# Performance work log

Hardware: AMD Instinct MI355X
Metric: run time of the kernel (lower is better)

## Reference

```python
import jax, jax.numpy as jnp
import numpy as np

K = 3  # n_neighbors


def setup_inputs() -> dict:
    key = jax.random.key(0)
    k1, k2, k3 = jax.random.split(key, 3)
    N, D, C, B = 400000, 27, 11, 512  # train size, 3*N_PEAKS_MAX, classes, query batch
    train_features = jax.random.normal(k1, (N, D), dtype=jnp.float32)
    label_idx = jax.random.randint(k2, (N,), 0, C)
    train_labels = jax.nn.one_hot(label_idx, C, dtype=jnp.float32)
    query = jax.random.normal(k3, (B, D), dtype=jnp.float32)
    return {"query": query, "train_features": train_features, "train_labels": train_labels}


def _divide_no_nan(x, y):
    # tf.math.divide_no_nan: 0 where denominator is 0
    y_safe = jnp.where(y != 0, y, 1.0)
    return jnp.where(y != 0, x / y_safe, 0.0)


def reference(query, train_features, train_labels):
    # scale = per-feature max abs over training set (computed in __init__)
    scale = jnp.max(jnp.abs(train_features), axis=0)            # [D]
    train_s = _divide_no_nan(train_features, scale)             # [N,D]
    q_s = _divide_no_nan(query, scale)                          # [B,D]

    xn = jnp.sum(train_s * train_s, axis=1)                     # [N]
    qn = jnp.sum(q_s * q_s, axis=1)                             # [B]
    d2 = qn[:, None] - 2.0 * jnp.einsum('bd,nd->bn', q_s, train_s) + xn[None, :]
    dist = jnp.sqrt(jnp.maximum(d2, 0.0))                       # [B,N]

    neg_kd, idx = jax.lax.top_k(-dist, K)                       # k smallest distances
    kd = -neg_kd                                                # [B,K]

    lab = train_labels[idx]                                     # [B,K,C]
    # inverse-distance weighted vote (safe against zero distances)
    kd_safe = jnp.where(kd == 0.0, 1.0, kd)
    votes = jnp.sum(lab / kd_safe[:, :, None], axis=1)          # [B,C]
    vote_res = jax.nn.one_hot(jnp.argmax(votes, axis=1), train_labels.shape[1], dtype=jnp.float32)

    # exact-match branch: if the nearest distance is 0, return its label directly
    zero_hit = (jnp.min(kd, axis=1) == 0.0)[:, None]            # [B,1]
    result = jnp.where(zero_hit, lab[:, 0, :], vote_res)        # [B,C]
    return kd, result
```

## Files before the change

### kernel.cpp

```cpp
#include <hip/hip_runtime.h>
#include <math.h>

typedef _Float16 h8 __attribute__((ext_vector_type(8)));
typedef float    f4v __attribute__((ext_vector_type(4)));

#define N_TRAIN 400000
#define DIMS    27
#define BQ      512
#define NCLS    11
#define KNN     3
#define NB      500
#define P1T     1024
#define PTS_BLK 800
#define PTS_SUP 160
#define NSUP    5
#define NPT     10
#define RAWF    4320
#define TILE_B  2048
#define NC      (NB * KNN)
#define SB      1024
#define RPB     392
#define SROWS   128
#define P2T     512

#define U64MAX 0xFFFFFFFFFFFFFFFFULL

__global__ __launch_bounds__(256) void k_scale(const float* __restrict__ train,
                                               unsigned* __restrict__ scale_u) {
    __shared__ float st[SROWS * DIMS];
    __shared__ float sp[243];
    int tid = threadIdx.x;
    int r0 = blockIdx.x * RPB;
    int r1 = min(r0 + RPB, N_TRAIN);
    int c  = tid % DIMS;
    int rr = tid / DIMS;
    float m = 0.f;
    for (int base = r0; base < r1; base += SROWS) {
        int cnt = min(SROWS, r1 - base);
        int tot4 = (cnt * DIMS) >> 2;
        const uint4* src4 = (const uint4*)(train + (size_t)base * DIMS);
        uint4* st4 = (uint4*)st;
        for (int i = tid; i < tot4; i += 256) st4[i] = src4[i];
        __syncthreads();
        if (tid < 243) {
            for (int r = rr; r < cnt; r += 9)
                m = fmaxf(m, fabsf(st[r * DIMS + c]));
        }
        __syncthreads();
    }
    if (tid < 243) sp[tid] = m;
    __syncthreads();
    if (tid < DIMS) {
        float v = 0.f;
#pragma unroll
        for (int g = 0; g < 9; ++g) v = fmaxf(v, sp[g * DIMS + tid]);
        atomicMax(&scale_u[tid], __float_as_uint(v));
    }
}

__global__ __launch_bounds__(64) void k_qprep(const float* __restrict__ query,
                                              const unsigned* __restrict__ scale_u,
                                              _Float16* __restrict__ Qhi,
                                              _Float16* __restrict__ Qlo) {
    int q = blockIdx.x * 64 + threadIdx.x;
    if (q >= BQ) return;
    const float* r = query + (size_t)q * DIMS;
#pragma unroll
    for (int d = 0; d < 32; ++d) {
        _Float16 hi = (_Float16)0.f, lo = (_Float16)0.f;
        if (d < DIMS) {
            float sc = __uint_as_float(scale_u[d]);
            float inv = (sc != 0.f) ? 1.f / sc : 0.f;
            float xs = r[d] * inv;
            hi = (_Float16)xs;
            lo = (_Float16)(xs - (float)hi);
        } else if (d == 27) {
            hi = (_Float16)1.f;
        }
        Qhi[q * 32 + d] = hi;
        Qlo[q * 32 + d] = lo;
    }
}

__device__ __forceinline__ void insert3(float d, int i, float* bd, int* bi) {
    if (d < bd[2] || (d == bd[2] && i < bi[2])) {
        if (d < bd[1] || (d == bd[1] && i < bi[1])) {
            bd[2] = bd[1]; bi[2] = bi[1];
            if (d < bd[0] || (d == bd[0] && i < bi[0])) {
                bd[1] = bd[0]; bi[1] = bi[0];
                bd[0] = d; bi[0] = i;
            } else { bd[1] = d; bi[1] = i; }
        } else { bd[2] = d; bi[2] = i; }
    }
}

__device__ __forceinline__ unsigned long long shfl_xor_u64(unsigned long long v, int m) {
    unsigned lo = (unsigned)v, hi = (unsigned)(v >> 32);
    lo = __shfl_xor(lo, m, 64);
    hi = __shfl_xor(hi, m, 64);
    return ((unsigned long long)hi << 32) | lo;
}

__device__ __forceinline__ void ins3u64(unsigned long long e,
                                        unsigned long long& t0,
                                        unsigned long long& t1,
                                        unsigned long long& t2) {
    unsigned long long a  = e < t2 ? e : t2;
    unsigned long long n2 = t1 > a ? t1 : a;
    unsigned long long n1 = t1 < a ? t1 : a;
    t2 = n2;
    unsigned long long m1 = t0 > n1 ? t0 : n1;
    t0 = t0 < n1 ? t0 : n1;
    t1 = m1;
}

__device__ __forceinline__ void stage16(const float* g, float* l) {
    __builtin_amdgcn_global_load_lds((const __attribute__((address_space(1))) void*)g,
                                     (__attribute__((address_space(3))) void*)l, 16, 0, 0);
}

__global__ __attribute__((amdgpu_flat_work_group_size(P1T, P1T)))
__attribute__((amdgpu_waves_per_eu(4)))
void k_pass1(const float* __restrict__ train,
             const unsigned* __restrict__ scale_u,
             const _Float16* __restrict__ Qhi,
             const _Float16* __restrict__ Qlo,
             unsigned long long* __restrict__ cand) {
    __shared__ float s_inv[32];
    __shared__ __align__(16) float raw[2][RAWF];
    __shared__ __align__(16) unsigned char conv[NPT * TILE_B];

    int tid = threadIdx.x;
    if (tid < 32) {
        float sc = __uint_as_float(scale_u[tid]);
        s_inv[tid] = (sc != 0.f) ? 1.f / sc : 0.f;
    }
    int lane = tid & 63, w = tid >> 6;
    int l15 = lane & 15, quad = lane >> 4;

    h8 bhi[2], blo[2];
#pragma unroll
    for (int j = 0; j < 2; ++j) {
        int qt = w * 2 + j;
        size_t e = (size_t)(qt * 16 + l15) * 32 + quad * 8;
        bhi[j] = *(const h8*)(Qhi + e);
        blo[j] = *(const h8*)(Qlo + e);
    }

    unsigned kb0[2][4], kb1[2][4];
#pragma unroll
    for (int j = 0; j < 2; ++j)
#pragma unroll
        for (int r = 0; r < 4; ++r) { kb0[j][r] = 0u; kb1[j][r] = 0u; }

    int p0 = blockIdx.x * PTS_BLK;
    const float* gsup = train + (size_t)p0 * DIMS;

    {
        const float* gp = gsup; float* lp = raw[0];
        stage16(gp + tid * 4, lp + tid * 4);
        if (tid < 56) stage16(gp + 4096 + tid * 4, lp + 4096 + tid * 4);
    }

    for (int s = 0; s < NSUP; ++s) {
        __syncthreads();

        const float* rw = raw[s & 1];
        if (tid < PTS_SUP * 4) {
            int p = tid >> 2, gq = tid & 3;
            float x[8]; float part = 0.f;
#pragma unroll
            for (int i = 0; i < 8; ++i) {
                int d = gq * 8 + i;
                int dc = d < DIMS ? d : (DIMS - 1);
                float v = rw[p * DIMS + dc] * s_inv[d];
                x[i] = v;
                part = fmaf(v, v, part);
            }
            part += __shfl_xor(part, 1, 64);
            part += __shfl_xor(part, 2, 64);
            h8 hv, lv;
#pragma unroll
            for (int i = 0; i < 8; ++i) {
                _Float16 h = (_Float16)x[i];
                hv[i] = h;
                lv[i] = (_Float16)(x[i] - (float)h);
            }
            if (gq == 3) {
                float tt = -0.5f * part;
                _Float16 th = (_Float16)tt;
                hv[3] = th;
                lv[3] = (_Float16)(tt - (float)th);
            }
            unsigned char* dstb = conv + (p >> 4) * TILE_B + gq * 256 + (p & 15) * 16;
            *(h8*)dstb = hv;
            *(h8*)(dstb + 1024) = lv;
        }
        __syncthreads();

        if (s + 1 < NSUP) {
            const float* gp = gsup + (size_t)(s + 1) * RAWF;
            float* lp = raw[(s + 1) & 1];
            stage16(gp + tid * 4, lp + tid * 4);
            if (tid < 56) stage16(gp + 4096 + tid * 4, lp + 4096 + tid * 4);
        }

        for (int t = 0; t < NPT; ++t) {
            const unsigned char* basep = conv + t * TILE_B;
            h8 ahi = *(const h8*)(basep + lane * 16);
            h8 alo = *(const h8*)(basep + 1024 + lane * 16);
            unsigned ic = 63u - (unsigned)(s * NPT + t);
#pragma unroll
            for (int j = 0; j < 2; ++j) {
                f4v acc = {64.f, 64.f, 64.f, 64.f};
                acc = __builtin_amdgcn_mfma_f32_16x16x32_f16(alo, bhi[j], acc, 0, 0, 0);
                acc = __builtin_amdgcn_mfma_f32_16x16x32_f16(ahi, blo[j], acc, 0, 0, 0);
                acc = __builtin_amdgcn_mfma_f32_16x16x32_f16(ahi, bhi[j], acc, 0, 0, 0);
#pragma unroll
                for (int r = 0; r < 4; ++r) {
                    unsigned key = (__float_as_uint(acc[r]) & 0xFFFFFFC0u) | ic;
                    unsigned b0 = kb0[j][r];
                    unsigned m  = key < b0 ? key : b0;
                    kb0[j][r]   = key > b0 ? key : b0;
                    unsigned b1 = kb1[j][r];
                    kb1[j][r]   = m > b1 ? m : b1;
                }
            }
        }
    }

    int g = blockIdx.x;
    int qr4 = quad * 4;
#pragma unroll
    for (int j = 0; j < 2; ++j) {
        unsigned long long t0 = U64MAX, t1 = U64MAX, t2 = U64MAX;
#pragma unroll
        for (int r = 0; r < 4; ++r) {
#pragma unroll
            for (int h = 0; h < 2; ++h) {
                unsigned k = h ? kb1[j][r] : kb0[j][r];
                unsigned tile = 63u - (k & 63u);
                unsigned gi = (unsigned)(p0 + (int)tile * 16 + qr4 + r);
                unsigned long long e = ((unsigned long long)(~(k | 63u)) << 32) | gi;
                ins3u64(e, t0, t1, t2);
            }
        }
#pragma unroll
        for (int step = 16; step <= 32; step <<= 1) {
            unsigned long long o0 = shfl_xor_u64(t0, step);
            unsigned long long o1 = shfl_xor_u64(t1, step);
            unsigned long long o2 = shfl_xor_u64(t2, step);
            ins3u64(o0, t0, t1, t2);
            ins3u64(o1, t0, t1, t2);
            ins3u64(o2, t0, t1, t2);
        }
        if (quad == 0) {
            int qq = (w * 2 + j) * 16 + l15;
            size_t off = (size_t)qq * NC + (size_t)g * KNN;
            cand[off + 0] = t0; cand[off + 1] = t1; cand[off + 2] = t2;
        }
    }
}

#define CE(a, b) do { unsigned long long lo_ = (a) < (b) ? (a) : (b); \
                      unsigned long long hi_ = (a) < (b) ? (b) : (a); \
                      (a) = lo_; (b) = hi_; } while (0)

__global__ __launch_bounds__(P2T) void k_pass2(const unsigned long long* __restrict__ cand,
                                               const float* __restrict__ train,
                                               const float* __restrict__ query,
                                               const unsigned* __restrict__ scale_u,
                                               const float* __restrict__ labels,
                                               float* __restrict__ out) {
    __shared__ unsigned long long smerge[64];
    int q = blockIdx.x;
    int tid = threadIdx.x, lane = tid & 63, w = tid >> 6;
    const unsigned long long* cd = cand + (size_t)q * NC;

    unsigned long long c0 = cd[tid];
    unsigned long long c1 = cd[tid + P2T];
    unsigned long long c2 = (tid + 2 * P2T < NC) ? cd[tid + 2 * P2T] : U64MAX;
    CE(c0, c1); CE(c0, c2); CE(c1, c2);

#pragma unroll
    for (int k = 0; k < 8; ++k) {
        unsigned long long m = c0;
#pragma unroll
        for (int st = 1; st < 64; st <<= 1) {
            unsigned long long o = shfl_xor_u64(m, st);
            if (o < m) m = o;
        }
        if (lane == 0) smerge[w * 8 + k] = m;
        bool win = (c0 == m);
        c0 = win ? c1 : c0;
        c1 = win ? c2 : c1;
        c2 = win ? U64MAX : c2;
    }
    __syncthreads();
    if (w != 0) return;

    int myi = 0x7fffffff;
    {
        unsigned long long cur = smerge[lane];
#pragma unroll
        for (int k = 0; k < 8; ++k) {
            unsigned long long m = cur;
#pragma unroll
            for (int st = 1; st < 64; st <<= 1) {
                unsigned long long o = shfl_xor_u64(m, st);
                if (o < m) m = o;
            }
            if (lane == k) myi = (int)(unsigned)m;
            if (cur == m) cur = U64MAX;
        }
    }

    float inv[DIMS], qs_[DIMS], qn_ = 0.f;
#pragma unroll
    for (int d = 0; d < DIMS; ++d) {
        float sc = __uint_as_float(scale_u[d]);
        float iv = (sc != 0.f) ? 1.f / sc : 0.f;
        float v = query[(size_t)q * DIMS + d] * iv;
        inv[d] = iv; qs_[d] = v;
        qn_ = fmaf(v, v, qn_);
    }

    float myd2 = 3.4e38f;
    if (lane < 8) {
        const float* r = train + (size_t)myi * DIMS;
        float xnv = 0.f, dot = 0.f;
#pragma unroll
        for (int d = 0; d < DIMS; ++d) {
            float v = r[d] * inv[d];
            xnv = fmaf(v, v, xnv);
            dot = fmaf(qs_[d], v, dot);
        }
        myd2 = fmaf(-2.f, dot, qn_ + xnv);
    }

    float bd[KNN] = {3.4e38f, 3.4e38f, 3.4e38f};
    int   bi[KNN] = {0x7fffffff, 0x7fffffff, 0x7fffffff};
#pragma unroll
    for (int k = 0; k < 8; ++k) {
        float dk = __shfl(myd2, k, 64);
        int   ik = __shfl(myi, k, 64);
        insert3(dk, ik, bd, bi);
    }

    if (lane == 0) {
        float kd[KNN];
#pragma unroll
        for (int k = 0; k < KNN; ++k) kd[k] = sqrtf(fmaxf(bd[k], 0.f));
        float lab[KNN][NCLS];
#pragma unroll
        for (int k = 0; k < KNN; ++k) {
            const float* lr = labels + (size_t)bi[k] * NCLS;
#pragma unroll
            for (int c = 0; c < NCLS; ++c) lab[k][c] = lr[c];
        }
        float votes[NCLS];
#pragma unroll
        for (int c = 0; c < NCLS; ++c) votes[c] = 0.f;
#pragma unroll
        for (int k = 0; k < KNN; ++k) {
            float ks = (kd[k] == 0.f) ? 1.f : kd[k];
#pragma unroll
            for (int c = 0; c < NCLS; ++c) votes[c] += lab[k][c] / ks;
        }
        int best = 0; float bv = votes[0];
#pragma unroll
        for (int c = 1; c < NCLS; ++c) { if (votes[c] > bv) { bv = votes[c]; best = c; } }
        bool zero_hit = (kd[0] == 0.f);
#pragma unroll
        for (int k = 0; k < KNN; ++k) out[(size_t)q * KNN + k] = kd[k];
        float* ro = out + (size_t)BQ * KNN + (size_t)q * NCLS;
#pragma unroll
        for (int c = 0; c < NCLS; ++c)
            ro[c] = zero_hit ? lab[0][c] : ((c == best) ? 1.f : 0.f);
    }
}

extern "C" void kernel_launch(void* const* d_in, const int* in_sizes, int n_in,
                              void* d_out, int out_size, void* d_ws, size_t ws_size,
                              hipStream_t stream) {
    const float* query  = (const float*)d_in[0];
    const float* train  = (const float*)d_in[1];
    const float* labels = (const float*)d_in[2];
    float* out = (float*)d_out;

    char* ws = (char*)d_ws;
    unsigned*  scale_u = (unsigned*)ws;
    _Float16*  Qhi = (_Float16*)(ws + 128);
    _Float16*  Qlo = (_Float16*)(ws + 32896);
    unsigned long long* cand = (unsigned long long*)(ws + 65664);

    hipMemsetAsync(ws, 0, 128, stream);
    k_scale<<<SB, 256, 0, stream>>>(train, scale_u);
    k_qprep<<<8, 64, 0, stream>>>(query, scale_u, Qhi, Qlo);
    k_pass1<<<NB, P1T, 0, stream>>>(train, scale_u, Qhi, Qlo, cand);
    k_pass2<<<BQ, P2T, 0, stream>>>(cand, train, query, scale_u, labels, out);
}
```

Baseline: 174.9 us.

## Double-buffer converted tiles to overlap conversion with MFMA scan of previous stage

Adds a second LDS buffer for the fp16 hi/lo converted training tiles. Each stage now converts super-tile s while running the MFMA distance and top-2 scan on super-tile s-1, with a final drain pass after the loop. This removes one block-wide barrier per stage and lets the convert ALU work interleave with matrix work. The global-to-LDS prefetch is also issued earlier in the stage. The cost is more LDS per block, which could reduce occupancy, plus extra code for the epilogue pass.

```diff
diff --git a/kernel.cpp b/kernel.cpp
--- a/kernel.cpp
+++ b/kernel.cpp
@@ -128,7 +128,7 @@
              unsigned long long* __restrict__ cand) {
     __shared__ float s_inv[32];
     __shared__ __align__(16) float raw[2][RAWF];
-    __shared__ __align__(16) unsigned char conv[NPT * TILE_B];
+    __shared__ __align__(16) unsigned char convb[2][NPT * TILE_B];
 
     int tid = threadIdx.x;
     if (tid < 32) {
@@ -153,6 +153,8 @@
 #pragma unroll
         for (int r = 0; r < 4; ++r) { kb0[j][r] = 0u; kb1[j][r] = 0u; }
 
+    const f4v z4 = {64.f, 64.f, 64.f, 64.f};
+
     int p0 = blockIdx.x * PTS_BLK;
     const float* gsup = train + (size_t)p0 * DIMS;
 
@@ -164,6 +166,13 @@
 
     for (int s = 0; s < NSUP; ++s) {
         __syncthreads();
+
+        if (s + 1 < NSUP) {
+            const float* gp = gsup + (size_t)(s + 1) * RAWF;
+            float* lp = raw[(s + 1) & 1];
+            stage16(gp + tid * 4, lp + tid * 4);
+            if (tid < 56) stage16(gp + 4096 + tid * 4, lp + 4096 + tid * 4);
+        }
 
         const float* rw = raw[s & 1];
         if (tid < PTS_SUP * 4) {
@@ -192,28 +201,52 @@
                 hv[3] = th;
                 lv[3] = (_Float16)(tt - (float)th);
             }
-            unsigned char* dstb = conv + (p >> 4) * TILE_B + gq * 256 + (p & 15) * 16;
+            unsigned char* dstb = convb[s & 1] + (p >> 4) * TILE_B + gq * 256 + (p & 15) * 16;
             *(h8*)dstb = hv;
             *(h8*)(dstb + 1024) = lv;
         }
-        __syncthreads();
-
-        if (s + 1 < NSUP) {
-            const float* gp = gsup + (size_t)(s + 1) * RAWF;
-            float* lp = raw[(s + 1) & 1];
-            stage16(gp + tid * 4, lp + tid * 4);
-            if (tid < 56) stage16(gp + 4096 + tid * 4, lp + 4096 + tid * 4);
-        }
-
+
+        if (s > 0) {
+            int ss = s - 1;
+            const unsigned char* cb = convb[ss & 1];
+            for (int t = 0; t < NPT; ++t) {
+                const unsigned char* basep = cb + t * TILE_B;
+                h8 ahi = *(const h8*)(basep + lane * 16);
+                h8 alo = *(const h8*)(basep + 1024 + lane * 16);
+                unsigned ic = 63u - (unsigned)(ss * NPT + t);
+#pragma unroll
+                for (int j = 0; j < 2; ++j) {
+                    f4v acc;
+                    acc = __builtin_amdgcn_mfma_f32_16x16x32_f16(alo, bhi[j], z4, 0, 0, 0);
+                    acc = __builtin_amdgcn_mfma_f32_16x16x32_f16(ahi, blo[j], acc, 0, 0, 0);
+                    acc = __builtin_amdgcn_mfma_f32_16x16x32_f16(ahi, bhi[j], acc, 0, 0, 0);
+#pragma unroll
+                    for (int r = 0; r < 4; ++r) {
+                        unsigned key = (__float_as_uint(acc[r]) & 0xFFFFFFC0u) | ic;
+                        unsigned b0 = kb0[j][r];
+                        unsigned m  = key < b0 ? key : b0;
+                        kb0[j][r]   = key > b0 ? key : b0;
+                        unsigned b1 = kb1[j][r];
+                        kb1[j][r]   = m > b1 ? m : b1;
+                    }
+                }
+            }
+        }
+    }
+
+    __syncthreads();
+    {
+        int ss = NSUP - 1;
+        const unsigned char* cb = convb[ss & 1];
         for (int t = 0; t < NPT; ++t) {
-            const unsigned char* basep = conv + t * TILE_B;
+            const unsigned char* basep = cb + t * TILE_B;
             h8 ahi = *(const h8*)(basep + lane * 16);
             h8 alo = *(const h8*)(basep + 1024 + lane * 16);
-            unsigned ic = 63u - (unsigned)(s * NPT + t);
+            unsigned ic = 63u - (unsigned)(ss * NPT + t);
 #pragma unroll
             for (int j = 0; j < 2; ++j) {
-                f4v acc = {64.f, 64.f, 64.f, 64.f};
-                acc = __builtin_amdgcn_mfma_f32_16x16x32_f16(alo, bhi[j], acc, 0, 0, 0);
+                f4v acc;
+                acc = __builtin_amdgcn_mfma_f32_16x16x32_f16(alo, bhi[j], z4, 0, 0, 0);
                 acc = __builtin_amdgcn_mfma_f32_16x16x32_f16(ahi, blo[j], acc, 0, 0, 0);
                 acc = __builtin_amdgcn_mfma_f32_16x16x32_f16(ahi, bhi[j], acc, 0, 0, 0);
 #pragma unroll
```

Result: no change. 175.9 us (+0.6%).
